# Optimization experiments

Measured on AMD Instinct MI355X. Metric: run time of the kernel, lower is better.

The kernel has to match this reference:

```python
import jax, jax.numpy as jnp
import numpy as np

B, C, H, W = 16, 512, 25, 25
HEADS = 8
HID = 2048
PATCH = 5  # hardcoded patch_size in FusionAttention
EPS_LN = 1e-5
EPS_BN = 1e-5


def _channel_layernorm(x, g, b):
    # torch: std = var(unbiased=False).sqrt(); (x-mean)/(std+eps)*g + b, over channel dim=1
    mean = jnp.mean(x, axis=1, keepdims=True)
    var = jnp.var(x, axis=1, keepdims=True)
    return (x - mean) / (jnp.sqrt(var) + EPS_LN) * g + b


def _dwconv3x3(x, w, b):
    # depthwise 3x3, padding 1; w: (C,1,3,3)
    y = jax.lax.conv_general_dilated(
        x, w, window_strides=(1, 1), padding=((1, 1), (1, 1)),
        feature_group_count=x.shape[1],
        dimension_numbers=('NCHW', 'OIHW', 'NCHW'))
    return y + b[None, :, None, None]


def setup_inputs() -> dict:
    key = jax.random.key(0)
    ks = jax.random.split(key, 20)
    s = 0.02
    d = {
        'x': jax.random.normal(ks[0], (B, C, H, W), jnp.float32),
        'ln1_g': jnp.ones((1, C, 1, 1), jnp.float32),
        'ln1_b': jnp.zeros((1, C, 1, 1), jnp.float32),
        'wq': jax.random.normal(ks[1], (C, 1, 3, 3), jnp.float32) * s,
        'bq': jnp.zeros((C,), jnp.float32),
        'wk': jax.random.normal(ks[2], (C, 1, 3, 3), jnp.float32) * s,
        'bk': jnp.zeros((C,), jnp.float32),
        'wv': jax.random.normal(ks[3], (C, 1, 3, 3), jnp.float32) * s,
        'bv': jnp.zeros((C,), jnp.float32),
        'swq': jax.random.normal(ks[4], (C, 1, 3, 3), jnp.float32) * s,
        'sbq': jnp.zeros((C,), jnp.float32),
        'swk': jax.random.normal(ks[5], (C, 1, 3, 3), jnp.float32) * s,
        'sbk': jnp.zeros((C,), jnp.float32),
        'swv': jax.random.normal(ks[6], (C, 1, 3, 3), jnp.float32) * s,
        'sbv': jnp.zeros((C,), jnp.float32),
        'proj_w': jax.random.normal(ks[7], (C, C, 1, 1), jnp.float32) * s,
        'bn_g': jnp.ones((C,), jnp.float32),
        'bn_b': jnp.zeros((C,), jnp.float32),
        'bn_mean': jnp.zeros((C,), jnp.float32),
        'bn_var': jnp.ones((C,), jnp.float32),
        'ln2_g': jnp.ones((1, C, 1, 1), jnp.float32),
        'ln2_b': jnp.zeros((1, C, 1, 1), jnp.float32),
        'w1': jax.random.normal(ks[8], (HID, C, 1, 1), jnp.float32) * s,
        'b1': jnp.zeros((HID,), jnp.float32),
        'w2': jax.random.normal(ks[9], (C, HID, 1, 1), jnp.float32) * s,
        'b2': jnp.zeros((C,), jnp.float32),
    }
    return d


def _fusion_attention(x, wq, bq, wk, bk, wv, bv, swq, sbq, swk, sbk, swv, sbv,
                      proj_w, bn_g, bn_b, bn_mean, bn_var):
    b, c, h, w = x.shape
    n = h * w
    hd = c // HEADS
    scale = hd ** -0.5

    def split_heads(t):  # (b,c,h,w) -> (b, heads, n, hd)
        return t.reshape(b, HEADS, hd, n).transpose(0, 1, 3, 2)

    q = split_heads(_dwconv3x3(x, wq, bq))
    k = split_heads(_dwconv3x3(x, wk, bk))
    v = split_heads(_dwconv3x3(x, wv, bv))

    dots = jnp.einsum('bhid,bhjd->bhij', q, k) * scale
    attn = jax.nn.softmax(dots, axis=-1)
    out = jnp.einsum('bhij,bhjd->bhid', attn, v)
    # rearrange 'b h (H W) d -> b (h d) H W' with H=PATCH
    out = out.transpose(0, 1, 3, 2).reshape(b, c, PATCH, n // PATCH)

    spe_q = _dwconv3x3(out, swq, sbq).reshape(b, c, n)          # b d (l w)
    spe_k = _dwconv3x3(out, swk, sbk).reshape(b, c, n).transpose(0, 2, 1)  # b (l w) d
    spe_v = _dwconv3x3(out, swv, sbv).reshape(b, c, n)

    attention = jax.nn.softmax(jnp.einsum('bcn,bnd->bcd', spe_q, spe_k) * scale, axis=-1)
    x_out = jnp.einsum('bcd,bdn->bcn', attention, spe_v).reshape(b, c, h, w)

    # 1x1 conv (no bias) + BatchNorm2d (eval mode)
    proj = jnp.einsum('oc,bchw->bohw', proj_w[:, :, 0, 0], x_out)
    proj = (proj - bn_mean[None, :, None, None]) / jnp.sqrt(bn_var + EPS_BN)[None, :, None, None]
    proj = proj * bn_g[None, :, None, None] + bn_b[None, :, None, None]
    return proj


def _feedforward(x, w1, b1, w2, b2):
    h1 = jnp.einsum('oc,bchw->bohw', w1[:, :, 0, 0], x) + b1[None, :, None, None]
    h1 = jax.nn.gelu(h1, approximate=False)
    return jnp.einsum('oc,bchw->bohw', w2[:, :, 0, 0], h1) + b2[None, :, None, None]


def reference(x, ln1_g, ln1_b, wq, bq, wk, bk, wv, bv, swq, sbq, swk, sbk,
              swv, sbv, proj_w, bn_g, bn_b, bn_mean, bn_var, ln2_g, ln2_b,
              w1, b1, w2, b2):
    y1 = x + _fusion_attention(_channel_layernorm(x, ln1_g, ln1_b),
                               wq, bq, wk, bk, wv, bv, swq, sbq, swk, sbk,
                               swv, sbv, proj_w, bn_g, bn_b, bn_mean, bn_var)
    y_out = y1 + _feedforward(_channel_layernorm(y1, ln2_g, ln2_b), w1, b1, w2, b2)
    return y_out
```

## Files before the change

### kernel.cpp

```cpp
#include <hip/hip_runtime.h>
#include <math.h>

constexpr int BATCH = 16;
constexpr int CH    = 512;
constexpr int NPIX  = 625;
constexpr int HEADS = 8;
constexpr int HDIM  = 64;
constexpr int HIDD  = 2048;

constexpr float EPS_LN = 1e-5f;
constexpr float EPS_BN = 1e-5f;
constexpr float SCALE  = 0.125f;

typedef __bf16 bf16x8 __attribute__((ext_vector_type(8)));
typedef float  f32x4  __attribute__((ext_vector_type(4)));

__global__ __launch_bounds__(256) void ln_kernel2(
    const float* __restrict__ x, const float* __restrict__ g,
    const float* __restrict__ bt, float* __restrict__ y) {
  __shared__ float ps[4][64];
  __shared__ float pss[4][64];
  int lane = threadIdx.x & 63;
  int w    = threadIdx.x >> 6;
  int b    = blockIdx.y;
  int i    = blockIdx.x * 64 + lane;
  int ic   = i < NPIX ? i : NPIX - 1;
  const float* xb = x + (size_t)b * CH * NPIX + ic;
  float s = 0.f, ss = 0.f;
  #pragma unroll 4
  for (int c = w * 128; c < w * 128 + 128; ++c) {
    float v = xb[(size_t)c * NPIX];
    s += v; ss += v * v;
  }
  ps[w][lane] = s; pss[w][lane] = ss;
  __syncthreads();
  float st  = ps[0][lane] + ps[1][lane] + ps[2][lane] + ps[3][lane];
  float sst = pss[0][lane] + pss[1][lane] + pss[2][lane] + pss[3][lane];
  float mean = st * (1.0f / CH);
  float var  = sst * (1.0f / CH) - mean * mean;
  float inv  = 1.0f / (sqrtf(fmaxf(var, 0.0f)) + EPS_LN);
  if (i >= NPIX) return;
  float* yb = y + (size_t)b * CH * NPIX + i;
  #pragma unroll 4
  for (int c = w * 128; c < w * 128 + 128; ++c) {
    float v = xb[(size_t)c * NPIX];
    yb[(size_t)c * NPIX] = (v - mean) * inv * g[c] + bt[c];
  }
}

__global__ void dwconv3_kernel(const float* __restrict__ src,
    const float* __restrict__ w0, const float* __restrict__ b0,
    const float* __restrict__ w1, const float* __restrict__ b1,
    const float* __restrict__ w2, const float* __restrict__ b2,
    float* __restrict__ d0, float* __restrict__ d1, float* __restrict__ d2,
    int Hc, int Wc) {
  size_t idx = (size_t)blockIdx.x * blockDim.x + threadIdx.x;
  size_t total = (size_t)BATCH * CH * Hc * Wc;
  if (idx >= total) return;
  int wp = (int)(idx % Wc);
  int hp = (int)((idx / Wc) % Hc);
  int c  = (int)((idx / ((size_t)Wc * Hc)) % CH);
  const float* f0 = w0 + c * 9;
  const float* f1 = w1 + c * 9;
  const float* f2 = w2 + c * 9;
  float a0 = 0.f, a1 = 0.f, a2 = 0.f;
  #pragma unroll
  for (int kh = -1; kh <= 1; ++kh) {
    int h2 = hp + kh; if (h2 < 0 || h2 >= Hc) continue;
    #pragma unroll
    for (int kw = -1; kw <= 1; ++kw) {
      int w2p = wp + kw; if (w2p < 0 || w2p >= Wc) continue;
      float v = src[idx + (size_t)kh * Wc + kw];
      int wi = (kh + 1) * 3 + (kw + 1);
      a0 += v * f0[wi]; a1 += v * f1[wi]; a2 += v * f2[wi];
    }
  }
  d0[idx] = a0 + b0[c];
  d1[idx] = a1 + b1[c];
  d2[idx] = a2 + b2[c];
}

__global__ void dwconv_spe_kernel(const float* __restrict__ src,
    const float* __restrict__ w0, const float* __restrict__ b0,
    const float* __restrict__ w1, const float* __restrict__ b1,
    const float* __restrict__ w2, const float* __restrict__ b2,
    __bf16* __restrict__ q16, __bf16* __restrict__ k16, float* __restrict__ v) {
  size_t idx = (size_t)blockIdx.x * blockDim.x + threadIdx.x;
  if (idx >= (size_t)BATCH * CH * 640) return;
  int n = (int)(idx % 640);
  int c = (int)((idx / 640) % CH);
  int b = (int)(idx / ((size_t)640 * CH));
  if (n >= NPIX) { q16[idx] = (__bf16)0.f; k16[idx] = (__bf16)0.f; return; }
  int hp = n / 125, wp = n % 125;
  size_t base = ((size_t)b * CH + c) * NPIX;
  const float* f0 = w0 + c * 9;
  const float* f1 = w1 + c * 9;
  const float* f2 = w2 + c * 9;
  float a0 = 0.f, a1 = 0.f, a2 = 0.f;
  #pragma unroll
  for (int kh = -1; kh <= 1; ++kh) {
    int h2 = hp + kh; if (h2 < 0 || h2 >= 5) continue;
    #pragma unroll
    for (int kw = -1; kw <= 1; ++kw) {
      int w2p = wp + kw; if (w2p < 0 || w2p >= 125) continue;
      float vv = src[base + h2 * 125 + w2p];
      int wi = (kh + 1) * 3 + (kw + 1);
      a0 += vv * f0[wi]; a1 += vv * f1[wi]; a2 += vv * f2[wi];
    }
  }
  q16[idx] = (__bf16)(a0 + b0[c]);
  k16[idx] = (__bf16)(a1 + b1[c]);
  v[base + n] = a2 + b2[c];
}

__global__ __launch_bounds__(256) void qk_to_bf16T(
    const float* __restrict__ q, const float* __restrict__ k,
    __bf16* __restrict__ qT, __bf16* __restrict__ kT) {
  __shared__ __bf16 tq[64][65];
  __shared__ __bf16 tk[64][65];
  int bh = blockIdx.y;
  int n0 = blockIdx.x * 64;
  int b = bh >> 3, h = bh & 7;
  const float* qb = q + (size_t)(b * CH + h * HDIM) * NPIX;
  const float* kb = k + (size_t)(b * CH + h * HDIM) * NPIX;
  #pragma unroll
  for (int it = 0; it < 16; ++it) {
    int idx = threadIdx.x + it * 256;
    int d = idx >> 6, n = idx & 63;
    int nn = n0 + n;
    float qv = (nn < NPIX) ? qb[(size_t)d * NPIX + nn] : 0.f;
    float kv = (nn < NPIX) ? kb[(size_t)d * NPIX + nn] : 0.f;
    tq[n][d] = (__bf16)qv;
    tk[n][d] = (__bf16)kv;
  }
  __syncthreads();
  size_t obase = (size_t)bh * NPIX;
  #pragma unroll
  for (int it = 0; it < 16; ++it) {
    int idx = threadIdx.x + it * 256;
    int n = idx >> 6, d = idx & 63;
    int nn = n0 + n;
    if (nn < NPIX) {
      qT[(obase + nn) * 64 + d] = tq[n][d];
      kT[(obase + nn) * 64 + d] = tk[n][d];
    }
  }
}

__global__ void v_to_bf16(const float* __restrict__ v, __bf16* __restrict__ v16) {
  int row = blockIdx.x;
  const float* src = v + (size_t)row * NPIX;
  __bf16* dst = v16 + (size_t)row * 640;
  for (int n = threadIdx.x; n < NPIX; n += 256) dst[n] = (__bf16)src[n];
}

__global__ __launch_bounds__(256) void head_attn_mfma3(
    const __bf16* __restrict__ qT, const __bf16* __restrict__ kT,
    const __bf16* __restrict__ vB, float* __restrict__ out) {
  __shared__ __align__(16) union SmU {
    unsigned char p[16 * 1296];
    float ostage[64][17];
  } sm;
  __shared__ float red_max[4][16];
  __shared__ float red_sum[4][16];

  int t = threadIdx.x;
  int w = t >> 6, lane = t & 63, g = lane >> 4, li = lane & 15;
  int h = blockIdx.y, b = blockIdx.z;
  int bh = b * HEADS + h;
  int i0 = blockIdx.x * 16;
  const __bf16* Qb = qT + (size_t)bh * NPIX * 64;
  const __bf16* Kb = kT + (size_t)bh * NPIX * 64;

  bf16x8 aq0, aq1;
  {
    int qr = i0 + li; if (qr > NPIX - 1) qr = NPIX - 1;
    const __bf16* qp = Qb + (size_t)qr * 64 + 8 * g;
    aq0 = *(const bf16x8*)(qp);
    aq1 = *(const bf16x8*)(qp + 32);
  }

  f32x4 s[10];
  #pragma unroll
  for (int cfl = 0; cfl < 10; ++cfl) {
    int kc = (w * 10 + cfl) * 16 + li;
    int kcl = kc > NPIX - 1 ? NPIX - 1 : kc;
    const __bf16* kp = Kb + (size_t)kcl * 64 + 8 * g;
    bf16x8 bk0 = *(const bf16x8*)(kp);
    bf16x8 bk1 = *(const bf16x8*)(kp + 32);
    f32x4 a = (f32x4){0.f, 0.f, 0.f, 0.f};
    a = __builtin_amdgcn_mfma_f32_16x16x32_bf16(aq0, bk0, a, 0, 0, 0);
    a = __builtin_amdgcn_mfma_f32_16x16x32_bf16(aq1, bk1, a, 0, 0, 0);
    s[cfl] = a * SCALE;
  }
  if (w == 3 && li > 0) {
    s[9][0] = -1e30f; s[9][1] = -1e30f; s[9][2] = -1e30f; s[9][3] = -1e30f;
  }

  #pragma unroll
  for (int r = 0; r < 4; ++r) {
    float mx = s[0][r];
    #pragma unroll
    for (int cfl = 1; cfl < 10; ++cfl) mx = fmaxf(mx, s[cfl][r]);
    mx = fmaxf(mx, __shfl_xor(mx, 1));
    mx = fmaxf(mx, __shfl_xor(mx, 2));
    mx = fmaxf(mx, __shfl_xor(mx, 4));
    mx = fmaxf(mx, __shfl_xor(mx, 8));
    if (li == 0) red_max[w][4 * g + r] = mx;
  }
  __syncthreads();

  #pragma unroll
  for (int r = 0; r < 4; ++r) {
    int row = 4 * g + r;
    float mx = fmaxf(fmaxf(red_max[0][row], red_max[1][row]),
                     fmaxf(red_max[2][row], red_max[3][row]));
    float sum = 0.f;
    #pragma unroll
    for (int cfl = 0; cfl < 10; ++cfl) {
      float p = __expf(s[cfl][r] - mx);
      s[cfl][r] = p;
      sum += p;
    }
    sum += __shfl_xor(sum, 1);
    sum += __shfl_xor(sum, 2);
    sum += __shfl_xor(sum, 4);
    sum += __shfl_xor(sum, 8);
    if (li == 0) red_sum[w][row] = sum;
  }
  __syncthreads();

  #pragma unroll
  for (int r = 0; r < 4; ++r) {
    int row = 4 * g + r;
    float l = red_sum[0][row] + red_sum[1][row] + red_sum[2][row] + red_sum[3][row];
    float inv = 1.0f / l;
    #pragma unroll
    for (int cfl = 0; cfl < 10; ++cfl) {
      int col = (w * 10 + cfl) * 16 + li;
      *(__bf16*)(&sm.p[row * 1296 + col * 2]) = (__bf16)(s[cfl][r] * inv);
    }
  }
  __syncthreads();

  const __bf16* vrow = vB + (size_t)(b * CH + h * HDIM + w * 16 + li) * 640;
  f32x4 o = (f32x4){0.f, 0.f, 0.f, 0.f};
  #pragma unroll
  for (int ks = 0; ks < 20; ++ks) {
    bf16x8 pa = *(const bf16x8*)(&sm.p[li * 1296 + ks * 64 + 16 * g]);
    bf16x8 bv = *(const bf16x8*)(vrow + ks * 32 + 8 * g);
    o = __builtin_amdgcn_mfma_f32_16x16x32_bf16(pa, bv, o, 0, 0, 0);
  }
  __syncthreads();

  #pragma unroll
  for (int r = 0; r < 4; ++r)
    sm.ostage[w * 16 + li][4 * g + r] = o[r];
  __syncthreads();
  size_t cbase = (size_t)(b * CH + h * HDIM);
  #pragma unroll
  for (int it = 0; it < 4; ++it) {
    int e = t + it * 256;
    int d = e >> 4, nl = e & 15;
    int n = i0 + nl;
    if (n < NPIX) out[(cbase + d) * NPIX + n] = sm.ostage[d][nl];
  }
}

__global__ __launch_bounds__(64) void chan_attn_mfma(
    const __bf16* __restrict__ sq, const __bf16* __restrict__ sk,
    __bf16* __restrict__ Am) {
  int lane = threadIdx.x & 63;
  int g = lane >> 4, li = lane & 15;
  int b = blockIdx.y;
  int cq0 = blockIdx.x * 16;
  const __bf16* qrow  = sq + ((size_t)b * CH + cq0 + li) * 640 + 8 * g;
  const __bf16* kbase = sk + ((size_t)b * CH + li) * 640 + 8 * g;
  f32x4 acc[32];
  #pragma unroll
  for (int i = 0; i < 32; ++i) acc[i] = (f32x4){0.f, 0.f, 0.f, 0.f};
  for (int ks = 0; ks < 20; ++ks) {
    bf16x8 af = *(const bf16x8*)(qrow + ks * 32);
    #pragma unroll
    for (int cf = 0; cf < 32; ++cf) {
      bf16x8 bfr = *(const bf16x8*)(kbase + (size_t)cf * 16 * 640 + ks * 32);
      acc[cf] = __builtin_amdgcn_mfma_f32_16x16x32_bf16(af, bfr, acc[cf], 0, 0, 0);
    }
  }
  #pragma unroll
  for (int i = 0; i < 32; ++i) acc[i] = acc[i] * SCALE;
  __bf16* Ab = Am + ((size_t)b * CH + cq0) * CH;
  #pragma unroll
  for (int r = 0; r < 4; ++r) {
    float mx = -1e30f;
    #pragma unroll
    for (int cf = 0; cf < 32; ++cf) mx = fmaxf(mx, acc[cf][r]);
    mx = fmaxf(mx, __shfl_xor(mx, 1));
    mx = fmaxf(mx, __shfl_xor(mx, 2));
    mx = fmaxf(mx, __shfl_xor(mx, 4));
    mx = fmaxf(mx, __shfl_xor(mx, 8));
    float sum = 0.f;
    #pragma unroll
    for (int cf = 0; cf < 32; ++cf) {
      float p = __expf(acc[cf][r] - mx);
      acc[cf][r] = p;
      sum += p;
    }
    sum += __shfl_xor(sum, 1);
    sum += __shfl_xor(sum, 2);
    sum += __shfl_xor(sum, 4);
    sum += __shfl_xor(sum, 8);
    float inv = 1.0f / sum;
    #pragma unroll
    for (int cf = 0; cf < 32; ++cf)
      Ab[(size_t)(4 * g + r) * CH + cf * 16 + li] = (__bf16)(acc[cf][r] * inv);
  }
}

template <int EPI>
__global__ __launch_bounds__(256) void gemm_nt(
    const __bf16* __restrict__ A, long long aBatch,
    const __bf16* __restrict__ B, long long bBatch,
    void* __restrict__ Cout, long long cBatch,
    int M, int N, int K,
    const float* __restrict__ p0, const float* __restrict__ p1,
    const float* __restrict__ res, long long resBatch) {
  __shared__ __align__(16) union {
    struct { unsigned char As[128 * 128]; unsigned char Bs[64 * 128]; } s;
    float Ce[4][64][17];
  } u;
  int t = threadIdx.x;
  int w = t >> 6, lane = t & 63, g = lane >> 4, li = lane & 15;
  int wm = w & 1, wn = w >> 1;
  int n0 = blockIdx.x * 64, m0 = blockIdx.y * 128, b = blockIdx.z;
  const __bf16* Ab = A + (size_t)b * aBatch;
  const __bf16* Bb = B + (size_t)b * bBatch;
  f32x4 acc[4][2];
  #pragma unroll
  for (int i = 0; i < 4; ++i)
    #pragma unroll
    for (int j = 0; j < 2; ++j) acc[i][j] = (f32x4){0.f, 0.f, 0.f, 0.f};

  for (int k0 = 0; k0 < K; k0 += 64) {
    bf16x8 ra[4], rb[2];
    #pragma unroll
    for (int i = 0; i < 4; ++i) {
      int e = t + i * 256;
      int row = e >> 3, cc = e & 7;
      int ar = m0 + row; ar = ar < M ? ar : M - 1;
      ra[i] = *(const bf16x8*)(Ab + (size_t)ar * K + k0 + cc * 8);
    }
    #pragma unroll
    for (int i = 0; i < 2; ++i) {
      int e = t + i * 256;
      int row = e >> 3, cc = e & 7;
      rb[i] = *(const bf16x8*)(Bb + (size_t)(n0 + row) * K + k0 + cc * 8);
    }
    __syncthreads();
    #pragma unroll
    for (int i = 0; i < 4; ++i) {
      int e = t + i * 256; int row = e >> 3, cc = e & 7;
      int off = (row * 128 + cc * 16) ^ ((row & 7) << 4);
      *(bf16x8*)(&u.s.As[off]) = ra[i];
    }
    #pragma unroll
    for (int i = 0; i < 2; ++i) {
      int e = t + i * 256; int row = e >> 3, cc = e & 7;
      int off = (row * 128 + cc * 16) ^ ((row & 7) << 4);
      *(bf16x8*)(&u.s.Bs[off]) = rb[i];
    }
    __syncthreads();
    #pragma unroll
    for (int ks = 0; ks < 2; ++ks) {
      bf16x8 af[4], bfr[2];
      #pragma unroll
      for (int mf = 0; mf < 4; ++mf) {
        int row = wm * 64 + mf * 16 + li;
        int off = (row * 128 + ks * 64 + g * 16) ^ ((row & 7) << 4);
        af[mf] = *(const bf16x8*)(&u.s.As[off]);
      }
      #pragma unroll
      for (int nf = 0; nf < 2; ++nf) {
        int row = wn * 32 + nf * 16 + li;
        int off = (row * 128 + ks * 64 + g * 16) ^ ((row & 7) << 4);
        bfr[nf] = *(const bf16x8*)(&u.s.Bs[off]);
      }
      #pragma unroll
      for (int mf = 0; mf < 4; ++mf)
        #pragma unroll
        for (int nf = 0; nf < 2; ++nf)
          acc[mf][nf] = __builtin_amdgcn_mfma_f32_16x16x32_bf16(
              af[mf], bfr[nf], acc[mf][nf], 0, 0, 0);
    }
    __syncthreads();
  }

  #pragma unroll
  for (int p = 0; p < 2; ++p) {
    __syncthreads();
    #pragma unroll
    for (int mf = 0; mf < 4; ++mf) {
      #pragma unroll
      for (int r = 0; r < 4; ++r)
        u.Ce[w][mf * 16 + 4 * g + r][li] = acc[mf][p][r];
    }
    __syncthreads();
    int m = m0 + wm * 64 + lane;
    int colb = n0 + wn * 32 + p * 16;
    if (m < M) {
      float vv[16];
      #pragma unroll
      for (int c = 0; c < 16; ++c) vv[c] = u.Ce[w][lane][c];
      if (EPI == 0) {
        __bf16* Cb = (__bf16*)Cout + (size_t)b * cBatch + (size_t)m * N + colb;
        bf16x8 o0, o1;
        #pragma unroll
        for (int j = 0; j < 8; ++j) { o0[j] = (__bf16)vv[j]; o1[j] = (__bf16)vv[8 + j]; }
        *(bf16x8*)(Cb) = o0;
        *(bf16x8*)(Cb + 8) = o1;
      } else if (EPI == 1) {
        float* Cf = (float*)Cout + (size_t)b * cBatch + (size_t)m * N + colb;
        const float* rp = res + (size_t)b * resBatch + (size_t)m * N + colb;
        #pragma unroll
        for (int c = 0; c < 16; ++c)
          vv[c] = vv[c] * p0[colb + c] + p1[colb + c] + rp[c];
        #pragma unroll
        for (int c4 = 0; c4 < 4; ++c4)
          *(f32x4*)(Cf + c4 * 4) = (f32x4){vv[c4*4], vv[c4*4+1], vv[c4*4+2], vv[c4*4+3]};
      } else if (EPI == 2) {
        __bf16* Cb = (__bf16*)Cout + (size_t)b * cBatch + (size_t)m * N + colb;
        #pragma unroll
        for (int c = 0; c < 16; ++c) {
          float xg = vv[c] + p0[colb + c];
          vv[c] = 0.5f * xg * (1.0f + erff(xg * 0.70710678118654752f));
        }
        bf16x8 o0, o1;
        #pragma unroll
        for (int j = 0; j < 8; ++j) { o0[j] = (__bf16)vv[j]; o1[j] = (__bf16)vv[8 + j]; }
        *(bf16x8*)(Cb) = o0;
        *(bf16x8*)(Cb + 8) = o1;
      } else {
        float* Cf = (float*)Cout + (size_t)b * cBatch + (size_t)m * N + colb;
        const float* rp = res + (size_t)b * resBatch + (size_t)m * N + colb;
        #pragma unroll
        for (int c = 0; c < 16; ++c)
          vv[c] = vv[c] + p0[colb + c] + rp[c];
        #pragma unroll
        for (int c4 = 0; c4 < 4; ++c4)
          *(f32x4*)(Cf + c4 * 4) = (f32x4){vv[c4*4], vv[c4*4+1], vv[c4*4+2], vv[c4*4+3]};
      }
    }
  }
}

template <typename TO>
__global__ __launch_bounds__(256) void transpose_bat(
    const float* __restrict__ in, TO* __restrict__ out, int R, int Cc) {
  __shared__ float tile[64][65];
  int b = blockIdx.z;
  int c0 = blockIdx.x * 64, r0 = blockIdx.y * 64;
  const float* ib = in + (size_t)b * R * Cc;
  TO* ob = out + (size_t)b * R * Cc;
  for (int e = threadIdx.x; e < 4096; e += 256) {
    int rr = e >> 6, cc = e & 63;
    int r = r0 + rr, c = c0 + cc;
    tile[rr][cc] = (r < R && c < Cc) ? ib[(size_t)r * Cc + c] : 0.f;
  }
  __syncthreads();
  for (int e = threadIdx.x; e < 4096; e += 256) {
    int cc = e >> 6, rr = e & 63;
    int r = r0 + rr, c = c0 + cc;
    if (r < R && c < Cc) ob[(size_t)c * R + r] = (TO)tile[rr][cc];
  }
}

__global__ __launch_bounds__(256) void ln2_row_kernel(
    const float* __restrict__ y, const float* __restrict__ g,
    const float* __restrict__ bt, __bf16* __restrict__ o) {
  int row = blockIdx.x * 4 + (threadIdx.x >> 6);
  int lane = threadIdx.x & 63;
  const float* yr = y + (size_t)row * CH + lane * 8;
  f32x4 v0 = *(const f32x4*)(yr);
  f32x4 v1 = *(const f32x4*)(yr + 4);
  float s = v0[0]+v0[1]+v0[2]+v0[3]+v1[0]+v1[1]+v1[2]+v1[3];
  float ss = v0[0]*v0[0]+v0[1]*v0[1]+v0[2]*v0[2]+v0[3]*v0[3]
           + v1[0]*v1[0]+v1[1]*v1[1]+v1[2]*v1[2]+v1[3]*v1[3];
  #pragma unroll
  for (int off = 32; off > 0; off >>= 1) {
    s  += __shfl_xor(s, off);
    ss += __shfl_xor(ss, off);
  }
  float mean = s * (1.0f / CH);
  float var  = ss * (1.0f / CH) - mean * mean;
  float inv  = 1.0f / (sqrtf(fmaxf(var, 0.0f)) + EPS_LN);
  f32x4 g0 = *(const f32x4*)(g + lane * 8);
  f32x4 g1 = *(const f32x4*)(g + lane * 8 + 4);
  f32x4 b0 = *(const f32x4*)(bt + lane * 8);
  f32x4 b1 = *(const f32x4*)(bt + lane * 8 + 4);
  bf16x8 ov;
  #pragma unroll
  for (int j = 0; j < 4; ++j) ov[j]     = (__bf16)((v0[j] - mean) * inv * g0[j] + b0[j]);
  #pragma unroll
  for (int j = 0; j < 4; ++j) ov[4 + j] = (__bf16)((v1[j] - mean) * inv * g1[j] + b1[j]);
  *(bf16x8*)(o + (size_t)row * CH + lane * 8) = ov;
}

__global__ void cast_bf16_kernel(const float* __restrict__ s, __bf16* __restrict__ d, int n) {
  int i = blockIdx.x * 256 + threadIdx.x;
  if (i < n) d[i] = (__bf16)s[i];
}

__global__ void bn_prep(const float* __restrict__ g, const float* __restrict__ bt,
                        const float* __restrict__ mean, const float* __restrict__ var,
                        float* __restrict__ scale, float* __restrict__ shift) {
  int c = blockIdx.x * blockDim.x + threadIdx.x;
  if (c >= CH) return;
  float s = g[c] * rsqrtf(var[c] + EPS_BN);
  scale[c] = s;
  shift[c] = bt[c] - mean[c] * s;
}

extern "C" void kernel_launch(void* const* d_in, const int* in_sizes, int n_in,
                              void* d_out, int out_size, void* d_ws, size_t ws_size,
                              hipStream_t stream) {
  const float* x      = (const float*)d_in[0];
  const float* ln1_g  = (const float*)d_in[1];
  const float* ln1_b  = (const float*)d_in[2];
  const float* wq     = (const float*)d_in[3];
  const float* bq     = (const float*)d_in[4];
  const float* wk     = (const float*)d_in[5];
  const float* bk     = (const float*)d_in[6];
  const float* wv     = (const float*)d_in[7];
  const float* bv     = (const float*)d_in[8];
  const float* swq    = (const float*)d_in[9];
  const float* sbq    = (const float*)d_in[10];
  const float* swk    = (const float*)d_in[11];
  const float* sbk    = (const float*)d_in[12];
  const float* swv    = (const float*)d_in[13];
  const float* sbv    = (const float*)d_in[14];
  const float* proj_w = (const float*)d_in[15];
  const float* bn_g   = (const float*)d_in[16];
  const float* bn_b   = (const float*)d_in[17];
  const float* bn_m   = (const float*)d_in[18];
  const float* bn_v   = (const float*)d_in[19];
  const float* ln2_g  = (const float*)d_in[20];
  const float* ln2_b  = (const float*)d_in[21];
  const float* w1     = (const float*)d_in[22];
  const float* b1     = (const float*)d_in[23];
  const float* w2     = (const float*)d_in[24];
  const float* b2     = (const float*)d_in[25];

  char* W = (char*)d_ws;
  const size_t SZB = 20480000;
  char* S0 = W;
  char* S1 = W + SZB;
  char* S2 = W + 2 * SZB;
  char* S3 = W + 3 * SZB;
  char* S4 = W + 4 * SZB;

  float*  xln   = (float*)S0;
  float*  qb    = (float*)S1;
  float*  kb    = (float*)S2;
  float*  vb    = (float*)S3;
  __bf16* qT    = (__bf16*)S0;
  __bf16* kTp   = qT + (size_t)BATCH * HEADS * NPIX * 64;
  __bf16* v16   = (__bf16*)d_out;
  float*  ab    = (float*)S4;
  __bf16* sq16  = (__bf16*)S1;
  __bf16* sk16  = (__bf16*)S2;
  float*  sv    = (float*)S3;
  __bf16* svT   = (__bf16*)S4;
  __bf16* Amat  = (__bf16*)S0;
  __bf16* pw16  = (__bf16*)(S0 + 10485760);
  __bf16* w116  = (__bf16*)(S0 + 10485760 + 524288);
  __bf16* w216  = (__bf16*)(S0 + 10485760 + 524288 + 2097152);
  float*  bnsc  = (float*)(S0 + 10485760 + 524288 + 2097152 + 2097152);
  float*  bnsh  = bnsc + CH;
  __bf16* xoutT = (__bf16*)S1;
  float*  x_nc  = (float*)S4;
  float*  y1_nc = (float*)S3;
  __bf16* y1ln  = (__bf16*)S0;
  __bf16* h1T   = (__bf16*)S1;
  float*  tmp_nc = (float*)S4;

  const size_t SZ = (size_t)BATCH * CH * NPIX;

  ln_kernel2<<<dim3(10, BATCH), 256, 0, stream>>>(x, ln1_g, ln1_b, xln);
  dwconv3_kernel<<<(int)((SZ + 255) / 256), 256, 0, stream>>>(
      xln, wq, bq, wk, bk, wv, bv, qb, kb, vb, 25, 25);
  qk_to_bf16T<<<dim3(10, BATCH * HEADS), 256, 0, stream>>>(qb, kb, qT, kTp);
  v_to_bf16<<<dim3(BATCH * CH), 256, 0, stream>>>(vb, v16);
  head_attn_mfma3<<<dim3(40, HEADS, BATCH), 256, 0, stream>>>(qT, kTp, v16, ab);
  dwconv_spe_kernel<<<(int)(((size_t)BATCH * CH * 640 + 255) / 256), 256, 0, stream>>>(
      ab, swq, sbq, swk, sbk, swv, sbv, sq16, sk16, sv);
  transpose_bat<__bf16><<<dim3(10, 8, BATCH), 256, 0, stream>>>(sv, svT, CH, NPIX);
  cast_bf16_kernel<<<1024, 256, 0, stream>>>(proj_w, pw16, CH * CH);
  cast_bf16_kernel<<<4096, 256, 0, stream>>>(w1, w116, HIDD * CH);
  cast_bf16_kernel<<<4096, 256, 0, stream>>>(w2, w216, CH * HIDD);
  bn_prep<<<2, 256, 0, stream>>>(bn_g, bn_b, bn_m, bn_v, bnsc, bnsh);
  chan_attn_mfma<<<dim3(32, BATCH), 64, 0, stream>>>(sq16, sk16, Amat);
  gemm_nt<0><<<dim3(8, 5, BATCH), 256, 0, stream>>>(
      svT, (long long)NPIX * CH, Amat, (long long)CH * CH,
      xoutT, (long long)NPIX * CH, NPIX, CH, CH,
      nullptr, nullptr, nullptr, 0);
  transpose_bat<float><<<dim3(10, 8, BATCH), 256, 0, stream>>>(x, x_nc, CH, NPIX);
  gemm_nt<1><<<dim3(8, 79, 1), 256, 0, stream>>>(
      xoutT, 0LL, pw16, 0LL, y1_nc, 0LL, BATCH * NPIX, CH, CH,
      bnsc, bnsh, x_nc, 0LL);
  ln2_row_kernel<<<BATCH * NPIX / 4, 256, 0, stream>>>(y1_nc, ln2_g, ln2_b, y1ln);
  gemm_nt<2><<<dim3(32, 79, 1), 256, 0, stream>>>(
      y1ln, 0LL, w116, 0LL, h1T, 0LL, BATCH * NPIX, HIDD, CH,
      b1, nullptr, nullptr, 0LL);
  gemm_nt<3><<<dim3(8, 79, 1), 256, 0, stream>>>(
      h1T, 0LL, w216, 0LL, tmp_nc, 0LL, BATCH * NPIX, CH, HIDD,
      b2, nullptr, y1_nc, 0LL);
  transpose_bat<float><<<dim3(8, 10, BATCH), 256, 0, stream>>>(
      tmp_nc, (float*)d_out, NPIX, CH);
}
```

Measured before the change: 592.6 us.

## Split channel attention across four waves and defer softmax normalization in head attention

The channel-attention kernel now runs 256 threads per block instead of one wave. Each wave computes 128 key columns and the softmax max and sum are reduced across waves through shared memory, which cuts per-thread accumulator registers from 32 to 8 fragments and adds parallelism. In head attention, the unnormalized probabilities are packed two bf16 values at a time via lane shuffles into 32-bit shared stores. The 1/sum scaling is moved after the PV MFMA, and two accumulators are used to shorten the MFMA dependency chain. The costs are extra syncthreads and shuffles, plus a small precision change from rounding unnormalized probabilities to bf16.

Measured after the change: 582.6 us. Within noise of the previous version (-1.7%).

```diff
diff --git a/kernel.cpp b/kernel.cpp
--- a/kernel.cpp
+++ b/kernel.cpp
@@ -14,6 +14,12 @@
 
 typedef __bf16 bf16x8 __attribute__((ext_vector_type(8)));
 typedef float  f32x4  __attribute__((ext_vector_type(4)));
+
+static __device__ inline unsigned pack_bf16(float lo, float hi) {
+  union { __bf16 h; unsigned short u; } a, b;
+  a.h = (__bf16)lo; b.h = (__bf16)hi;
+  return ((unsigned)b.u << 16) | (unsigned)a.u;
+}
 
 __global__ __launch_bounds__(256) void ln_kernel2(
     const float* __restrict__ x, const float* __restrict__ g,
@@ -154,7 +160,7 @@
   for (int n = threadIdx.x; n < NPIX; n += 256) dst[n] = (__bf16)src[n];
 }
 
-__global__ __launch_bounds__(256) void head_attn_mfma3(
+__global__ __launch_bounds__(256) void head_attn_mfma4(
     const __bf16* __restrict__ qT, const __bf16* __restrict__ kT,
     const __bf16* __restrict__ vB, float* __restrict__ out) {
   __shared__ __align__(16) union SmU {
@@ -231,25 +237,42 @@
   __syncthreads();
 
   #pragma unroll
+  for (int cfp = 0; cfp < 5; ++cfp) {
+    int cf0 = 2 * cfp, cf1 = cf0 + 1;
+    #pragma unroll
+    for (int r = 0; r < 4; ++r) {
+      float v0 = s[cf0][r], v1 = s[cf1][r];
+      float t0 = __shfl_xor(v0, 1);
+      float t1 = __shfl_xor(v1, 1);
+      bool even = (li & 1) == 0;
+      float lo = even ? v0 : t1;
+      float hi = even ? t0 : v1;
+      int col = even ? ((w * 10 + cf0) * 16 + li)
+                     : ((w * 10 + cf1) * 16 + li - 1);
+      int row = 4 * g + r;
+      *(unsigned*)(&sm.p[row * 1296 + col * 2]) = pack_bf16(lo, hi);
+    }
+  }
+  __syncthreads();
+
+  const __bf16* vrow = vB + (size_t)(b * CH + h * HDIM + w * 16 + li) * 640;
+  f32x4 oa = (f32x4){0.f, 0.f, 0.f, 0.f};
+  f32x4 ob = (f32x4){0.f, 0.f, 0.f, 0.f};
+  #pragma unroll
+  for (int ks = 0; ks < 20; ks += 2) {
+    bf16x8 pa0 = *(const bf16x8*)(&sm.p[li * 1296 + ks * 64 + 16 * g]);
+    bf16x8 bv0 = *(const bf16x8*)(vrow + ks * 32 + 8 * g);
+    oa = __builtin_amdgcn_mfma_f32_16x16x32_bf16(pa0, bv0, oa, 0, 0, 0);
+    bf16x8 pa1 = *(const bf16x8*)(&sm.p[li * 1296 + (ks + 1) * 64 + 16 * g]);
+    bf16x8 bv1 = *(const bf16x8*)(vrow + (ks + 1) * 32 + 8 * g);
+    ob = __builtin_amdgcn_mfma_f32_16x16x32_bf16(pa1, bv1, ob, 0, 0, 0);
+  }
+  f32x4 o = oa + ob;
+  #pragma unroll
   for (int r = 0; r < 4; ++r) {
     int row = 4 * g + r;
     float l = red_sum[0][row] + red_sum[1][row] + red_sum[2][row] + red_sum[3][row];
-    float inv = 1.0f / l;
-    #pragma unroll
-    for (int cfl = 0; cfl < 10; ++cfl) {
-      int col = (w * 10 + cfl) * 16 + li;
-      *(__bf16*)(&sm.p[row * 1296 + col * 2]) = (__bf16)(s[cfl][r] * inv);
-    }
-  }
-  __syncthreads();
-
-  const __bf16* vrow = vB + (size_t)(b * CH + h * HDIM + w * 16 + li) * 640;
-  f32x4 o = (f32x4){0.f, 0.f, 0.f, 0.f};
-  #pragma unroll
-  for (int ks = 0; ks < 20; ++ks) {
-    bf16x8 pa = *(const bf16x8*)(&sm.p[li * 1296 + ks * 64 + 16 * g]);
-    bf16x8 bv = *(const bf16x8*)(vrow + ks * 32 + 8 * g);
-    o = __builtin_amdgcn_mfma_f32_16x16x32_bf16(pa, bv, o, 0, 0, 0);
+    o[r] *= (1.0f / l);
   }
   __syncthreads();
 
@@ -267,53 +290,73 @@
   }
 }
 
-__global__ __launch_bounds__(64) void chan_attn_mfma(
+__global__ __launch_bounds__(256) void chan_attn_mfma2(
     const __bf16* __restrict__ sq, const __bf16* __restrict__ sk,
     __bf16* __restrict__ Am) {
-  int lane = threadIdx.x & 63;
-  int g = lane >> 4, li = lane & 15;
+  __shared__ float red_max[4][16];
+  __shared__ float red_sum[4][16];
+  int t = threadIdx.x;
+  int w = t >> 6, lane = t & 63, g = lane >> 4, li = lane & 15;
   int b = blockIdx.y;
   int cq0 = blockIdx.x * 16;
   const __bf16* qrow  = sq + ((size_t)b * CH + cq0 + li) * 640 + 8 * g;
-  const __bf16* kbase = sk + ((size_t)b * CH + li) * 640 + 8 * g;
-  f32x4 acc[32];
-  #pragma unroll
-  for (int i = 0; i < 32; ++i) acc[i] = (f32x4){0.f, 0.f, 0.f, 0.f};
+  const __bf16* kbase = sk + ((size_t)b * CH + w * 128 + li) * 640 + 8 * g;
+  f32x4 acc[8];
+  #pragma unroll
+  for (int i = 0; i < 8; ++i) acc[i] = (f32x4){0.f, 0.f, 0.f, 0.f};
   for (int ks = 0; ks < 20; ++ks) {
     bf16x8 af = *(const bf16x8*)(qrow + ks * 32);
     #pragma unroll
-    for (int cf = 0; cf < 32; ++cf) {
-      bf16x8 bfr = *(const bf16x8*)(kbase + (size_t)cf * 16 * 640 + ks * 32);
-      acc[cf] = __builtin_amdgcn_mfma_f32_16x16x32_bf16(af, bfr, acc[cf], 0, 0, 0);
-    }
-  }
-  #pragma unroll
-  for (int i = 0; i < 32; ++i) acc[i] = acc[i] * SCALE;
-  __bf16* Ab = Am + ((size_t)b * CH + cq0) * CH;
+    for (int cfl = 0; cfl < 8; ++cfl) {
+      bf16x8 bfr = *(const bf16x8*)(kbase + (size_t)cfl * 16 * 640 + ks * 32);
+      acc[cfl] = __builtin_amdgcn_mfma_f32_16x16x32_bf16(af, bfr, acc[cfl], 0, 0, 0);
+    }
+  }
+  #pragma unroll
+  for (int i = 0; i < 8; ++i) acc[i] = acc[i] * SCALE;
+
   #pragma unroll
   for (int r = 0; r < 4; ++r) {
-    float mx = -1e30f;
-    #pragma unroll
-    for (int cf = 0; cf < 32; ++cf) mx = fmaxf(mx, acc[cf][r]);
+    float mx = acc[0][r];
+    #pragma unroll
+    for (int cfl = 1; cfl < 8; ++cfl) mx = fmaxf(mx, acc[cfl][r]);
     mx = fmaxf(mx, __shfl_xor(mx, 1));
     mx = fmaxf(mx, __shfl_xor(mx, 2));
     mx = fmaxf(mx, __shfl_xor(mx, 4));
     mx = fmaxf(mx, __shfl_xor(mx, 8));
+    if (li == 0) red_max[w][4 * g + r] = mx;
+  }
+  __syncthreads();
+
+  #pragma unroll
+  for (int r = 0; r < 4; ++r) {
+    int row = 4 * g + r;
+    float mx = fmaxf(fmaxf(red_max[0][row], red_max[1][row]),
+                     fmaxf(red_max[2][row], red_max[3][row]));
     float sum = 0.f;
     #pragma unroll
-    for (int cf = 0; cf < 32; ++cf) {
-      float p = __expf(acc[cf][r] - mx);
-      acc[cf][r] = p;
+    for (int cfl = 0; cfl < 8; ++cfl) {
+      float p = __expf(acc[cfl][r] - mx);
+      acc[cfl][r] = p;
       sum += p;
     }
     sum += __shfl_xor(sum, 1);
     sum += __shfl_xor(sum, 2);
     sum += __shfl_xor(sum, 4);
     sum += __shfl_xor(sum, 8);
-    float inv = 1.0f / sum;
-    #pragma unroll
-    for (int cf = 0; cf < 32; ++cf)
-      Ab[(size_t)(4 * g + r) * CH + cf * 16 + li] = (__bf16)(acc[cf][r] * inv);
+    if (li == 0) red_sum[w][row] = sum;
+  }
+  __syncthreads();
+
+  __bf16* Ab = Am + ((size_t)b * CH + cq0) * CH + w * 128;
+  #pragma unroll
+  for (int r = 0; r < 4; ++r) {
+    int row = 4 * g + r;
+    float l = red_sum[0][row] + red_sum[1][row] + red_sum[2][row] + red_sum[3][row];
+    float inv = 1.0f / l;
+    #pragma unroll
+    for (int cfl = 0; cfl < 8; ++cfl)
+      Ab[(size_t)row * CH + cfl * 16 + li] = (__bf16)(acc[cfl][r] * inv);
   }
 }
 
@@ -590,7 +633,7 @@
       xln, wq, bq, wk, bk, wv, bv, qb, kb, vb, 25, 25);
   qk_to_bf16T<<<dim3(10, BATCH * HEADS), 256, 0, stream>>>(qb, kb, qT, kTp);
   v_to_bf16<<<dim3(BATCH * CH), 256, 0, stream>>>(vb, v16);
-  head_attn_mfma3<<<dim3(40, HEADS, BATCH), 256, 0, stream>>>(qT, kTp, v16, ab);
+  head_attn_mfma4<<<dim3(40, HEADS, BATCH), 256, 0, stream>>>(qT, kTp, v16, ab);
   dwconv_spe_kernel<<<(int)(((size_t)BATCH * CH * 640 + 255) / 256), 256, 0, stream>>>(
       ab, swq, sbq, swk, sbk, swv, sbv, sq16, sk16, sv);
   transpose_bat<__bf16><<<dim3(10, 8, BATCH), 256, 0, stream>>>(sv, svT, CH, NPIX);
@@ -598,7 +641,7 @@
   cast_bf16_kernel<<<4096, 256, 0, stream>>>(w1, w116, HIDD * CH);
   cast_bf16_kernel<<<4096, 256, 0, stream>>>(w2, w216, CH * HIDD);
   bn_prep<<<2, 256, 0, stream>>>(bn_g, bn_b, bn_m, bn_v, bnsc, bnsh);
-  chan_attn_mfma<<<dim3(32, BATCH), 64, 0, stream>>>(sq16, sk16, Amat);
+  chan_attn_mfma2<<<dim3(32, BATCH), 256, 0, stream>>>(sq16, sk16, Amat);
   gemm_nt<0><<<dim3(8, 5, BATCH), 256, 0, stream>>>(
       svT, (long long)NPIX * CH, Amat, (long long)CH * CH,
       xoutT, (long long)NPIX * CH, NPIX, CH, CH,
```
